# Kernel optimization log

Hardware: AMD Instinct MI355X
Metric: run time of the kernel (lower is better)

Reference implementation:

```python
import jax, jax.numpy as jnp
import numpy as np

N, D, H, O, E = 4096, 1024, 4096, 1024, 8
TOP_K = 2

def setup_inputs() -> dict:
    key = jax.random.key(0)
    k = jax.random.split(key, 4)
    x  = jax.random.normal(k[0], (N, D), dtype=jnp.float32)
    Wg = jax.random.normal(k[1], (D, E), dtype=jnp.float32) * (1.0 / np.sqrt(D))
    W1 = jax.random.normal(k[2], (E, D, H), dtype=jnp.float32) * (1.0 / np.sqrt(D))
    b1 = jnp.zeros((E, H), dtype=jnp.float32)
    W2 = jax.random.normal(k[3], (E, H, O), dtype=jnp.float32) * (1.0 / np.sqrt(H))
    b2 = jnp.zeros((E, O), dtype=jnp.float32)
    return {"x": x, "Wg": Wg, "W1": W1, "b1": b1, "W2": W2, "b2": b2}

def reference(x, Wg, W1, b1, W2, b2):
    # Gate: Linear(bias=False) -> ReLU (lin() appends act) -> softmax
    logits = jax.nn.relu(x @ Wg)                      # [N, E]
    probs = jax.nn.softmax(logits, axis=1)            # [N, E]
    top_p, sel = jax.lax.top_k(probs, TOP_K)          # [N, K]
    top_p = top_p / jnp.sum(top_p, axis=-1, keepdims=True)
    # Per-token combine weights over experts: [N, E]
    combine = jnp.sum(jax.nn.one_hot(sel, E, dtype=x.dtype) * top_p[..., None], axis=1)
    # Experts: ReLU(x W1 + b1) -> ReLU(h W2 + b2); final ReLU because lin() adds act on output layer
    h = jax.nn.relu(jnp.einsum('nd,edh->enh', x, W1) + b1[:, None, :])   # [E, N, H]
    y = jax.nn.relu(jnp.einsum('enh,eho->eno', h, W2) + b2[:, None, :])  # [E, N, O]
    out = jnp.einsum('eno,ne->no', y, combine)                            # [N, O]
    return out
```

## Files before the change

### kernel.cpp

```cpp
#include <hip/hip_runtime.h>
#include <cstdint>

#define NTOK 4096
#define DDIM 1024
#define HDIM 4096
#define ODIM 1024
#define NEXP 8
#define NSLOT (2*NTOK)
#define MAXTILES 72

typedef __bf16 bf16x8 __attribute__((ext_vector_type(8)));
typedef float  f32x4  __attribute__((ext_vector_type(4)));
typedef unsigned short ushort8v __attribute__((ext_vector_type(8)));

__device__ __forceinline__ unsigned short f2bf(float f) {
    union { float f; unsigned int u; } v; v.f = f;
    unsigned int r = (v.u + 0x7FFF + ((v.u >> 16) & 1)) >> 16;
    return (unsigned short)r;
}

typedef const void __attribute__((address_space(1)))* gas_ptr;
typedef void       __attribute__((address_space(3)))* las_ptr;

__global__ void gate_kernel(const float* __restrict__ x, const float* __restrict__ Wg,
                            int2* __restrict__ sel, float2* __restrict__ wts,
                            int* __restrict__ counts) {
    int wave = threadIdx.x >> 6;
    int lane = threadIdx.x & 63;
    int n = blockIdx.x * 4 + wave;
    float acc[NEXP];
#pragma unroll
    for (int e = 0; e < NEXP; e++) acc[e] = 0.f;
    const float* xr = x + (size_t)n * DDIM;
    for (int i = 0; i < DDIM / 64; i++) {
        int d = i * 64 + lane;
        float xv = xr[d];
        const float* wr = Wg + d * NEXP;
#pragma unroll
        for (int e = 0; e < NEXP; e++) acc[e] = fmaf(xv, wr[e], acc[e]);
    }
#pragma unroll
    for (int e = 0; e < NEXP; e++) {
#pragma unroll
        for (int off = 32; off >= 1; off >>= 1)
            acc[e] += __shfl_xor(acc[e], off, 64);
    }
    if (lane == 0) {
        float l0 = -1e30f, l1 = -1e30f; int e0 = 0, e1 = 0;
#pragma unroll
        for (int e = 0; e < NEXP; e++) {
            float v = fmaxf(acc[e], 0.f);
            if (v > l0)      { l1 = l0; e1 = e0; l0 = v; e0 = e; }
            else if (v > l1) { l1 = v;  e1 = e; }
        }
        float w0 = 1.f / (1.f + expf(l1 - l0));
        sel[n] = make_int2(e0, e1);
        wts[n] = make_float2(w0, 1.f - w0);
        atomicAdd(&counts[e0], 1);
        atomicAdd(&counts[e1], 1);
    }
}

__global__ void scan_kernel(const int* __restrict__ counts, int* __restrict__ offsets,
                            int* __restrict__ cursor, int4* __restrict__ tile_meta,
                            int* __restrict__ ntiles) {
    if (threadIdx.x == 0 && blockIdx.x == 0) {
        int s = 0, t = 0;
        for (int e = 0; e < NEXP; e++) {
            offsets[e] = s; cursor[e] = s;
            int c = counts[e];
            for (int r = 0; r < c; r += 128)
                tile_meta[t++] = make_int4(e, s + r, min(128, c - r), 0);
            s += c;
        }
        offsets[NEXP] = s;
        *ntiles = t;
    }
}

__global__ void assign_kernel(const int2* __restrict__ sel, const float2* __restrict__ wts,
                              int* __restrict__ cursor,
                              int* __restrict__ slot_token, float* __restrict__ slot_weight) {
    int n = blockIdx.x * blockDim.x + threadIdx.x;
    if (n >= NTOK) return;
    int2 s = sel[n]; float2 w = wts[n];
    int p0 = atomicAdd(&cursor[s.x], 1);
    slot_token[p0] = n; slot_weight[p0] = w.x;
    int p1 = atomicAdd(&cursor[s.y], 1);
    slot_token[p1] = n; slot_weight[p1] = w.y;
}

__global__ void cast_x_kernel(const float* __restrict__ x, unsigned short* __restrict__ xb) {
    int i = blockIdx.x * blockDim.x + threadIdx.x;
    float4 v = ((const float4*)x)[i];
    ushort4 o;
    o.x = f2bf(v.x); o.y = f2bf(v.y); o.z = f2bf(v.z); o.w = f2bf(v.w);
    ((ushort4*)xb)[i] = o;
}

__global__ void transpose_cast_kernel(const float* __restrict__ src, unsigned short* __restrict__ dst,
                                      int R, int C) {
    __shared__ float tile[64][65];
    int e = blockIdx.z;
    const float* s = src + (size_t)e * R * C;
    unsigned short* d = dst + (size_t)e * R * C;
    int t = threadIdx.x;
    int r0 = blockIdx.y * 64, c0 = blockIdx.x * 64;
#pragma unroll
    for (int p = 0; p < 4; p++) {
        int r = p * 16 + (t >> 4);
        int c = (t & 15) * 4;
        float4 v = *(const float4*)&s[(size_t)(r0 + r) * C + (c0 + c)];
        tile[r][c] = v.x; tile[r][c + 1] = v.y; tile[r][c + 2] = v.z; tile[r][c + 3] = v.w;
    }
    __syncthreads();
    int c = t >> 2, rb = (t & 3) * 16;
#pragma unroll
    for (int j = 0; j < 2; j++) {
        ushort8v v;
#pragma unroll
        for (int i = 0; i < 8; i++) v[i] = f2bf(tile[rb + j * 8 + i][c]);
        *(ushort8v*)&d[(size_t)(c0 + c) * R + (r0 + rb + j * 8)] = v;
    }
}

template <int MODE, int KDIM, int NDIM>
__global__ __launch_bounds__(256) void moe_gemm_kernel(
    const unsigned short* __restrict__ A,
    const unsigned short* __restrict__ B,
    const float* __restrict__ bias,
    const int4* __restrict__ tile_meta,
    const int* __restrict__ ntiles,
    const int* __restrict__ slot_token,
    const float* __restrict__ slot_weight,
    unsigned short* __restrict__ h,
    float* __restrict__ out) {

    if ((int)blockIdx.x >= *ntiles) return;
    int4 tm = tile_meta[blockIdx.x];
    int e = tm.x, slotBase = tm.y, rows = tm.z;
    int colBase = blockIdx.y * 128;

    __shared__ __align__(16) unsigned short As[128 * 64];
    __shared__ __align__(16) unsigned short Bs[128 * 64];

    int tid = threadIdx.x;
    int w = tid >> 6, l = tid & 63;
    int quad = l >> 4, lr = l & 15;
    int wm = w & 1, wn = w >> 1;
    int lr8 = l >> 3, u = l & 7;
    int gu = u ^ lr8;

    const unsigned short* ag[4];
    const unsigned short* bg[4];
    const unsigned short* Be = B + (size_t)e * NDIM * KDIM;
#pragma unroll
    for (int j = 0; j < 4; j++) {
        int r = 32 * w + 8 * j + lr8;
        int slot = min(slotBase + r, NSLOT - 1);
        if constexpr (MODE == 1) {
            int tok = slot_token[slot];
            ag[j] = A + (size_t)tok * KDIM + gu * 8;
        } else {
            ag[j] = A + (size_t)slot * KDIM + gu * 8;
        }
        bg[j] = Be + (size_t)(colBase + r) * KDIM + gu * 8;
    }

    unsigned short* AsW = As + 32 * w * 64;
    unsigned short* BsW = Bs + 32 * w * 64;

    f32x4 zero = {0.f, 0.f, 0.f, 0.f};
    f32x4 acc[4][4];
#pragma unroll
    for (int m = 0; m < 4; m++)
#pragma unroll
        for (int n = 0; n < 4; n++) acc[m][n] = zero;

    int swz = (lr & 7);
    for (int k0 = 0; k0 < KDIM; k0 += 64) {
#pragma unroll
        for (int j = 0; j < 4; j++)
            __builtin_amdgcn_global_load_lds((gas_ptr)(ag[j] + k0), (las_ptr)(AsW + j * 512), 16, 0, 0);
#pragma unroll
        for (int j = 0; j < 4; j++)
            __builtin_amdgcn_global_load_lds((gas_ptr)(bg[j] + k0), (las_ptr)(BsW + j * 512), 16, 0, 0);
        __syncthreads();
#pragma unroll
        for (int ks = 0; ks < 2; ks++) {
            int su = ((ks * 4 + quad) ^ swz) * 8;
            bf16x8 af[4], bf[4];
#pragma unroll
            for (int m = 0; m < 4; m++)
                af[m] = *(const bf16x8*)&As[(wm * 64 + m * 16 + lr) * 64 + su];
#pragma unroll
            for (int n = 0; n < 4; n++)
                bf[n] = *(const bf16x8*)&Bs[(wn * 64 + n * 16 + lr) * 64 + su];
#pragma unroll
            for (int m = 0; m < 4; m++)
#pragma unroll
                for (int n = 0; n < 4; n++)
                    acc[m][n] = __builtin_amdgcn_mfma_f32_16x16x32_bf16(af[m], bf[n], acc[m][n], 0, 0, 0);
        }
        __syncthreads();
    }

    if constexpr (MODE == 1) {
        const float* bv = bias + e * NDIM;
#pragma unroll
        for (int n = 0; n < 4; n++) {
            int gc = colBase + wn * 64 + n * 16 + lr;
            float b = bv[gc];
#pragma unroll
            for (int m = 0; m < 4; m++) {
                int rloc = wm * 64 + m * 16 + quad * 4;
#pragma unroll
                for (int i = 0; i < 4; i++) {
                    int r = rloc + i;
                    if (r < rows) {
                        float v = fmaxf(acc[m][n][i] + b, 0.f);
                        h[(size_t)(slotBase + r) * NDIM + gc] = f2bf(v);
                    }
                }
            }
        }
    } else {
        const float* bv = bias + e * NDIM;
#pragma unroll
        for (int m = 0; m < 4; m++) {
            int rloc = wm * 64 + m * 16 + quad * 4;
#pragma unroll
            for (int i = 0; i < 4; i++) {
                int r = rloc + i;
                if (r >= rows) continue;
                int s = slotBase + r;
                int tok = slot_token[s];
                float wgt = slot_weight[s];
                float* orow = out + (size_t)tok * ODIM;
#pragma unroll
                for (int n = 0; n < 4; n++) {
                    int gc = colBase + wn * 64 + n * 16 + lr;
                    float v = fmaxf(acc[m][n][i] + bv[gc], 0.f) * wgt;
                    atomicAdd(&orow[gc], v);
                }
            }
        }
    }
}

extern "C" void kernel_launch(void* const* d_in, const int* in_sizes, int n_in,
                              void* d_out, int out_size, void* d_ws, size_t ws_size,
                              hipStream_t stream) {
    const float* x  = (const float*)d_in[0];
    const float* Wg = (const float*)d_in[1];
    const float* W1 = (const float*)d_in[2];
    const float* b1 = (const float*)d_in[3];
    const float* W2 = (const float*)d_in[4];
    const float* b2 = (const float*)d_in[5];
    float* out = (float*)d_out;

    char* ws = (char*)d_ws;
    int*    counts      = (int*)(ws + 0);
    int*    cursor      = (int*)(ws + 64);
    int*    offsets     = (int*)(ws + 128);
    int*    ntiles      = (int*)(ws + 192);
    int4*   tile_meta   = (int4*)(ws + 256);
    int2*   sel         = (int2*)(ws + 2048);
    float2* wts         = (float2*)(ws + 34816);
    int*    slot_token  = (int*)(ws + 67584);
    float*  slot_weight = (float*)(ws + 100352);
    unsigned short* xb  = (unsigned short*)(ws + 2097152);
    unsigned short* W1T = (unsigned short*)(ws + 10485760);
    unsigned short* W2T = (unsigned short*)(ws + 77594624);
    unsigned short* hbf = (unsigned short*)(ws + 144703488);

    hipMemsetAsync(d_out, 0, (size_t)NTOK * ODIM * sizeof(float), stream);
    hipMemsetAsync(ws, 0, 256, stream);

    gate_kernel<<<NTOK / 4, 256, 0, stream>>>(x, Wg, sel, wts, counts);
    scan_kernel<<<1, 64, 0, stream>>>(counts, offsets, cursor, tile_meta, ntiles);
    assign_kernel<<<NTOK / 256, 256, 0, stream>>>(sel, wts, cursor, slot_token, slot_weight);

    cast_x_kernel<<<(NTOK * DDIM / 4) / 256, 256, 0, stream>>>(x, xb);
    transpose_cast_kernel<<<dim3(HDIM / 64, DDIM / 64, NEXP), 256, 0, stream>>>(W1, W1T, DDIM, HDIM);
    transpose_cast_kernel<<<dim3(ODIM / 64, HDIM / 64, NEXP), 256, 0, stream>>>(W2, W2T, HDIM, ODIM);

    moe_gemm_kernel<1, DDIM, HDIM><<<dim3(MAXTILES, HDIM / 128), 256, 0, stream>>>(
        xb, W1T, b1, tile_meta, ntiles, slot_token, slot_weight, hbf, nullptr);
    moe_gemm_kernel<2, HDIM, ODIM><<<dim3(MAXTILES, ODIM / 128), 256, 0, stream>>>(
        hbf, W2T, b2, tile_meta, ntiles, slot_token, slot_weight, nullptr, out);
}
```

Measured before the change: 806.5 us.

## Double-buffer MoE GEMM LDS, swap grid order, fuse cast and routing kernels

The grouped GEMM now double-buffers its A/B LDS tiles. It issues the next k-slice's global-to-LDS loads before computing the current one, using a partial vmcnt wait and raw barriers, so memory latency overlaps MFMA work. The grid is transposed so consecutive blocks share a token tile and walk output columns, which changes L2 reuse of the gathered A rows. The x-to-bf16 cast is folded into the gate kernel, and the scan and assign kernels are merged into one single-block route kernel using LDS atomics, which removes launches. LDS use doubles, and the single-block routing serializes slot assignment.

```diff
diff --git a/kernel.cpp b/kernel.cpp
--- a/kernel.cpp
+++ b/kernel.cpp
@@ -24,7 +24,7 @@
 
 __global__ void gate_kernel(const float* __restrict__ x, const float* __restrict__ Wg,
                             int2* __restrict__ sel, float2* __restrict__ wts,
-                            int* __restrict__ counts) {
+                            int* __restrict__ counts, unsigned short* __restrict__ xb) {
     int wave = threadIdx.x >> 6;
     int lane = threadIdx.x & 63;
     int n = blockIdx.x * 4 + wave;
@@ -32,9 +32,11 @@
 #pragma unroll
     for (int e = 0; e < NEXP; e++) acc[e] = 0.f;
     const float* xr = x + (size_t)n * DDIM;
+    unsigned short* xbr = xb + (size_t)n * DDIM;
     for (int i = 0; i < DDIM / 64; i++) {
         int d = i * 64 + lane;
         float xv = xr[d];
+        xbr[d] = f2bf(xv);
         const float* wr = Wg + d * NEXP;
 #pragma unroll
         for (int e = 0; e < NEXP; e++) acc[e] = fmaf(xv, wr[e], acc[e]);
@@ -61,41 +63,32 @@
     }
 }
 
-__global__ void scan_kernel(const int* __restrict__ counts, int* __restrict__ offsets,
-                            int* __restrict__ cursor, int4* __restrict__ tile_meta,
-                            int* __restrict__ ntiles) {
-    if (threadIdx.x == 0 && blockIdx.x == 0) {
-        int s = 0, t = 0;
+__global__ void route_kernel(const int2* __restrict__ sel, const float2* __restrict__ wts,
+                             const int* __restrict__ counts, int* __restrict__ offsets,
+                             int4* __restrict__ tile_meta, int* __restrict__ ntiles,
+                             int* __restrict__ slot_token, float* __restrict__ slot_weight) {
+    __shared__ int cur[NEXP];
+    int t = threadIdx.x;
+    if (t == 0) {
+        int s = 0, nt = 0;
         for (int e = 0; e < NEXP; e++) {
-            offsets[e] = s; cursor[e] = s;
+            offsets[e] = s; cur[e] = s;
             int c = counts[e];
             for (int r = 0; r < c; r += 128)
-                tile_meta[t++] = make_int4(e, s + r, min(128, c - r), 0);
+                tile_meta[nt++] = make_int4(e, s + r, min(128, c - r), 0);
             s += c;
         }
         offsets[NEXP] = s;
-        *ntiles = t;
-    }
-}
-
-__global__ void assign_kernel(const int2* __restrict__ sel, const float2* __restrict__ wts,
-                              int* __restrict__ cursor,
-                              int* __restrict__ slot_token, float* __restrict__ slot_weight) {
-    int n = blockIdx.x * blockDim.x + threadIdx.x;
-    if (n >= NTOK) return;
-    int2 s = sel[n]; float2 w = wts[n];
-    int p0 = atomicAdd(&cursor[s.x], 1);
-    slot_token[p0] = n; slot_weight[p0] = w.x;
-    int p1 = atomicAdd(&cursor[s.y], 1);
-    slot_token[p1] = n; slot_weight[p1] = w.y;
-}
-
-__global__ void cast_x_kernel(const float* __restrict__ x, unsigned short* __restrict__ xb) {
-    int i = blockIdx.x * blockDim.x + threadIdx.x;
-    float4 v = ((const float4*)x)[i];
-    ushort4 o;
-    o.x = f2bf(v.x); o.y = f2bf(v.y); o.z = f2bf(v.z); o.w = f2bf(v.w);
-    ((ushort4*)xb)[i] = o;
+        *ntiles = nt;
+    }
+    __syncthreads();
+    for (int n = t; n < NTOK; n += blockDim.x) {
+        int2 se = sel[n]; float2 w = wts[n];
+        int p0 = atomicAdd(&cur[se.x], 1);
+        slot_token[p0] = n; slot_weight[p0] = w.x;
+        int p1 = atomicAdd(&cur[se.y], 1);
+        slot_token[p1] = n; slot_weight[p1] = w.y;
+    }
 }
 
 __global__ void transpose_cast_kernel(const float* __restrict__ src, unsigned short* __restrict__ dst,
@@ -136,13 +129,13 @@
     unsigned short* __restrict__ h,
     float* __restrict__ out) {
 
-    if ((int)blockIdx.x >= *ntiles) return;
-    int4 tm = tile_meta[blockIdx.x];
+    if ((int)blockIdx.y >= *ntiles) return;
+    int4 tm = tile_meta[blockIdx.y];
     int e = tm.x, slotBase = tm.y, rows = tm.z;
-    int colBase = blockIdx.y * 128;
-
-    __shared__ __align__(16) unsigned short As[128 * 64];
-    __shared__ __align__(16) unsigned short Bs[128 * 64];
+    int colBase = blockIdx.x * 128;
+
+    __shared__ __align__(16) unsigned short As[2][128 * 64];
+    __shared__ __align__(16) unsigned short Bs[2][128 * 64];
 
     int tid = threadIdx.x;
     int w = tid >> 6, l = tid & 63;
@@ -167,9 +160,6 @@
         bg[j] = Be + (size_t)(colBase + r) * KDIM + gu * 8;
     }
 
-    unsigned short* AsW = As + 32 * w * 64;
-    unsigned short* BsW = Bs + 32 * w * 64;
-
     f32x4 zero = {0.f, 0.f, 0.f, 0.f};
     f32x4 acc[4][4];
 #pragma unroll
@@ -178,32 +168,50 @@
         for (int n = 0; n < 4; n++) acc[m][n] = zero;
 
     int swz = (lr & 7);
-    for (int k0 = 0; k0 < KDIM; k0 += 64) {
+    constexpr int NI = KDIM / 64;
+
+    auto issue = [&](int k, int s) {
+        unsigned short* AsW = &As[s][32 * w * 64];
+        unsigned short* BsW = &Bs[s][32 * w * 64];
 #pragma unroll
         for (int j = 0; j < 4; j++)
-            __builtin_amdgcn_global_load_lds((gas_ptr)(ag[j] + k0), (las_ptr)(AsW + j * 512), 16, 0, 0);
+            __builtin_amdgcn_global_load_lds((gas_ptr)(ag[j] + k * 64), (las_ptr)(AsW + j * 512), 16, 0, 0);
 #pragma unroll
         for (int j = 0; j < 4; j++)
-            __builtin_amdgcn_global_load_lds((gas_ptr)(bg[j] + k0), (las_ptr)(BsW + j * 512), 16, 0, 0);
-        __syncthreads();
+            __builtin_amdgcn_global_load_lds((gas_ptr)(bg[j] + k * 64), (las_ptr)(BsW + j * 512), 16, 0, 0);
+    };
+    auto compute = [&](int s) {
+        const unsigned short* A_ = As[s];
+        const unsigned short* B_ = Bs[s];
 #pragma unroll
         for (int ks = 0; ks < 2; ks++) {
             int su = ((ks * 4 + quad) ^ swz) * 8;
             bf16x8 af[4], bf[4];
 #pragma unroll
             for (int m = 0; m < 4; m++)
-                af[m] = *(const bf16x8*)&As[(wm * 64 + m * 16 + lr) * 64 + su];
+                af[m] = *(const bf16x8*)&A_[(wm * 64 + m * 16 + lr) * 64 + su];
 #pragma unroll
             for (int n = 0; n < 4; n++)
-                bf[n] = *(const bf16x8*)&Bs[(wn * 64 + n * 16 + lr) * 64 + su];
+                bf[n] = *(const bf16x8*)&B_[(wn * 64 + n * 16 + lr) * 64 + su];
 #pragma unroll
             for (int m = 0; m < 4; m++)
 #pragma unroll
                 for (int n = 0; n < 4; n++)
                     acc[m][n] = __builtin_amdgcn_mfma_f32_16x16x32_bf16(af[m], bf[n], acc[m][n], 0, 0, 0);
         }
-        __syncthreads();
-    }
+    };
+
+    issue(0, 0);
+    for (int k = 0; k < NI - 1; k++) {
+        issue(k + 1, (k + 1) & 1);
+        asm volatile("s_waitcnt vmcnt(8)" ::: "memory");
+        asm volatile("s_barrier" ::: "memory");
+        compute(k & 1);
+        asm volatile("s_barrier" ::: "memory");
+    }
+    asm volatile("s_waitcnt vmcnt(0)" ::: "memory");
+    asm volatile("s_barrier" ::: "memory");
+    compute((NI - 1) & 1);
 
     if constexpr (MODE == 1) {
         const float* bv = bias + e * NDIM;
@@ -261,7 +269,6 @@
 
     char* ws = (char*)d_ws;
     int*    counts      = (int*)(ws + 0);
-    int*    cursor      = (int*)(ws + 64);
     int*    offsets     = (int*)(ws + 128);
     int*    ntiles      = (int*)(ws + 192);
     int4*   tile_meta   = (int4*)(ws + 256);
@@ -277,16 +284,15 @@
     hipMemsetAsync(d_out, 0, (size_t)NTOK * ODIM * sizeof(float), stream);
     hipMemsetAsync(ws, 0, 256, stream);
 
-    gate_kernel<<<NTOK / 4, 256, 0, stream>>>(x, Wg, sel, wts, counts);
-    scan_kernel<<<1, 64, 0, stream>>>(counts, offsets, cursor, tile_meta, ntiles);
-    assign_kernel<<<NTOK / 256, 256, 0, stream>>>(sel, wts, cursor, slot_token, slot_weight);
-
-    cast_x_kernel<<<(NTOK * DDIM / 4) / 256, 256, 0, stream>>>(x, xb);
+    gate_kernel<<<NTOK / 4, 256, 0, stream>>>(x, Wg, sel, wts, counts, xb);
+    route_kernel<<<1, 512, 0, stream>>>(sel, wts, counts, offsets, tile_meta, ntiles,
+                                        slot_token, slot_weight);
+
     transpose_cast_kernel<<<dim3(HDIM / 64, DDIM / 64, NEXP), 256, 0, stream>>>(W1, W1T, DDIM, HDIM);
     transpose_cast_kernel<<<dim3(ODIM / 64, HDIM / 64, NEXP), 256, 0, stream>>>(W2, W2T, HDIM, ODIM);
 
-    moe_gemm_kernel<1, DDIM, HDIM><<<dim3(MAXTILES, HDIM / 128), 256, 0, stream>>>(
+    moe_gemm_kernel<1, DDIM, HDIM><<<dim3(HDIM / 128, MAXTILES), 256, 0, stream>>>(
         xb, W1T, b1, tile_meta, ntiles, slot_token, slot_weight, hbf, nullptr);
-    moe_gemm_kernel<2, HDIM, ODIM><<<dim3(MAXTILES, ODIM / 128), 256, 0, stream>>>(
+    moe_gemm_kernel<2, HDIM, ODIM><<<dim3(ODIM / 128, MAXTILES), 256, 0, stream>>>(
         hbf, W2T, b2, tile_meta, ntiles, slot_token, slot_weight, nullptr, out);
 }
```

After: 775.3 us. 1.04x faster.
